# Kernel tuning notes

Measured on AMD Instinct MI355X. Metric: run time of the kernel, lower is better.

## Reference

```python
import jax, jax.numpy as jnp
import numpy as np

N = 100_000   # nodes
E = 1_600_000 # edges
IN = 128
OUT = 64
L = 3         # n_layers


def setup_inputs() -> dict:
    key = jax.random.key(0)
    ks = jax.random.split(key, 4)
    x = jax.random.normal(ks[0], (N, IN), dtype=jnp.float32)
    edge_index = jax.random.randint(ks[1], (2, E), 0, N, dtype=jnp.int64)
    # Glorot-ish init like torch Linear default
    s0 = 1.0 / np.sqrt(IN)
    W0 = jax.random.uniform(ks[2], (IN, OUT), jnp.float32, -s0, s0)
    b0 = jnp.zeros((OUT,), jnp.float32)
    so = 1.0 / np.sqrt(OUT)
    Ws = jax.random.uniform(ks[3], (L - 1, OUT, OUT), jnp.float32, -so, so)
    bs = jnp.zeros((L - 1, OUT), jnp.float32)
    return {"x": x, "edge_index": edge_index, "W0": W0, "b0": b0, "Ws": Ws, "bs": bs}


def _gcn_conv(x, src, dst, norm, W, b):
    # dense transform then degree-normalized scatter-add over edges (incl. self-loops)
    h = x @ W                                  # [N, out]
    msg = h[src] * norm[:, None]               # [E+N, out]
    out = jax.ops.segment_sum(msg, dst, num_segments=N)
    return out + b


def reference(x, edge_index, W0, b0, Ws, bs):
    loops = jnp.arange(N, dtype=edge_index.dtype)
    src = jnp.concatenate([edge_index[0], loops])  # source nodes (x_j)
    dst = jnp.concatenate([edge_index[1], loops])  # aggregation targets
    # symmetric GCN normalization: deg over A+I, norm = d^-1/2[src]*d^-1/2[dst]
    deg = jax.ops.segment_sum(jnp.ones(src.shape, x.dtype), dst, num_segments=N)
    dinv = jnp.where(deg > 0, jax.lax.rsqrt(deg), jnp.zeros((), x.dtype))
    norm = dinv[src] * dinv[dst]

    x_temp = _gcn_conv(x, src, dst, norm, W0, b0)
    h = x_temp
    for i in range(L - 1):  # fixed small layer loop
        h = jax.nn.relu(_gcn_conv(h, src, dst, norm, Ws[i], bs[i]))
    return h + x_temp  # sum_res residual
```

## Files before the change

kernel.cpp:

```cpp
#include <hip/hip_runtime.h>


#define LB 8
#define BKN 256
#define CHUNK 4096
#define EPT 16
#define CAP 8192
#define PADS 3
#define CAPCOL (CAP + BKN * PADS)

typedef unsigned short ushort_t;
typedef __attribute__((ext_vector_type(8))) short bf16x8;
typedef __attribute__((ext_vector_type(4))) float f32x4;

__device__ __forceinline__ unsigned f2bf(float f) {
    unsigned u = __builtin_bit_cast(unsigned, f);
    return (u + 0x7FFFu + ((u >> 16) & 1u)) >> 16;
}
__device__ __forceinline__ float bf2f(ushort_t h) {
    unsigned u = ((unsigned)h) << 16;
    return __builtin_bit_cast(float, u);
}
__device__ __forceinline__ float bflo(unsigned u) {
    return __builtin_bit_cast(float, u << 16);
}
__device__ __forceinline__ float bfhi(unsigned u) {
    return __builtin_bit_cast(float, u & 0xFFFF0000u);
}

__device__ int detect_f64(const int* ei, int E, int* sflag) {
    if (threadIdx.x == 0) *sflag = 0;
    __syncthreads();
    const unsigned* raw = (const unsigned*)ei;
    int dwords = min(2 * E, 512);
    int any = 0;
    for (int i = threadIdx.x; i < dwords; i += blockDim.x)
        if ((i & 1) && raw[i]) any = 1;
    if (any) atomicOr(sflag, 1);
    __syncthreads();
    return !*sflag;
}

__global__ __launch_bounds__(256) void k_scatter(
        const int* __restrict__ ei, int E,
        int* __restrict__ bucketCursor, unsigned int* __restrict__ packed) {
    __shared__ int hist[512];
    __shared__ int base[512];
    __shared__ int sflag;
    int f64 = detect_f64(ei, E, &sflag);
    int b0 = blockIdx.x * CHUNK;
    int n = min(CHUNK, E - b0);
    int tid = threadIdx.x;
    for (int i = tid; i < 512; i += 256) hist[i] = 0;
    __syncthreads();
    int dreg[EPT], sreg[EPT];
#pragma unroll
    for (int i = 0; i < EPT; i++) {
        int idx = tid + i * 256;
        if (idx < n) {
            int e = b0 + idx;
            dreg[i] = f64 ? ei[2 * (E + e)] : ei[E + e];
            sreg[i] = f64 ? ei[2 * e] : ei[e];
            atomicAdd(&hist[dreg[i] >> LB], 1);
        }
    }
    __syncthreads();
    for (int i = tid; i < 512; i += 256) {
        int c = hist[i];
        base[i] = c ? atomicAdd(&bucketCursor[i], c) : 0;
        hist[i] = 0;
    }
    __syncthreads();
#pragma unroll
    for (int i = 0; i < EPT; i++) {
        int idx = tid + i * 256;
        if (idx < n) {
            int bk = dreg[i] >> LB;
            int pos = bk * CAP + base[bk] + atomicAdd(&hist[bk], 1);
            packed[pos] = ((unsigned)sreg[i] << LB) | (unsigned)(dreg[i] & (BKN - 1));
        }
    }
}

__global__ __launch_bounds__(256) void k_sort(
        const unsigned int* __restrict__ packed, const int* __restrict__ bucketCursor,
        int* __restrict__ col, int2* __restrict__ rp2, float* __restrict__ dinv,
        ushort_t* __restrict__ hs, int N) {
    __shared__ int hist[BKN];
    __shared__ int s[BKN];
    __shared__ int cur[BKN];
    int tid = threadIdx.x;
    int b = blockIdx.x;
    int start = b * CAP;
    int end = start + bucketCursor[b];
    hist[tid] = 0;
    __syncthreads();
    for (int e = start + tid; e < end; e += 256)
        atomicAdd(&hist[packed[e] & (BKN - 1)], 1);
    __syncthreads();
    int v = hist[tid];
    int pv = (v + PADS) & ~PADS;
    s[tid] = pv;
    __syncthreads();
    for (int off = 1; off < 256; off <<= 1) {
        int x = (tid >= off) ? s[tid - off] : 0;
        __syncthreads();
        if (tid >= off) s[tid] += x;
        __syncthreads();
    }
    int excl = s[tid] - pv;
    int st = b * CAPCOL + excl;
    cur[tid] = st;
    int node = (b << LB) + tid;
    if (node < N) {
        rp2[node] = make_int2(st, st + pv);
        dinv[node] = rsqrtf((float)(v + 1));
        for (int i = v; i < pv; i++) col[st + i] = N;
    }
    if (b == 0 && tid < 64) hs[(size_t)N * 64 + tid] = 0;
    __syncthreads();
    for (int e = start + tid; e < end; e += 256) {
        unsigned pvk = packed[e];
        int pos = atomicAdd(&cur[pvk & (BKN - 1)], 1);
        col[pos] = (int)(pvk >> LB);
    }
}

__global__ __launch_bounds__(256) void k_gemm1(
        const float* __restrict__ A, const float* __restrict__ W,
        const float* __restrict__ dinv, ushort_t* __restrict__ out, int nrows) {
    const int K = 128;
    __shared__ ushort_t sWT[64 * (K + 8)];
    int tid = threadIdx.x;
    for (int i = tid; i < K * 64; i += 256) {
        int n = i & 63, k = i >> 6;
        sWT[n * (K + 8) + k] = (ushort_t)f2bf(W[i]);
    }
    __syncthreads();
    int wave = tid >> 6, lane = tid & 63;
    int quad = lane >> 4, l16 = lane & 15;
    int rowBase = blockIdx.x * 128 + wave * 32;
    f32x4 acc[2][4];
#pragma unroll
    for (int r = 0; r < 2; r++)
#pragma unroll
        for (int c = 0; c < 4; c++) acc[r][c] = (f32x4){0.f, 0.f, 0.f, 0.f};
#pragma unroll
    for (int chunk = 0; chunk < K / 32; chunk++) {
        bf16x8 afr[2];
#pragma unroll
        for (int r = 0; r < 2; r++) {
            int row = rowBase + r * 16 + l16;
            if (row >= nrows) row = nrows - 1;
            const float* ap = A + (size_t)row * K + chunk * 32 + quad * 8;
            float4 v0 = *(const float4*)ap;
            float4 v1 = *(const float4*)(ap + 4);
            bf16x8 a;
            a[0] = (short)f2bf(v0.x); a[1] = (short)f2bf(v0.y);
            a[2] = (short)f2bf(v0.z); a[3] = (short)f2bf(v0.w);
            a[4] = (short)f2bf(v1.x); a[5] = (short)f2bf(v1.y);
            a[6] = (short)f2bf(v1.z); a[7] = (short)f2bf(v1.w);
            afr[r] = a;
        }
#pragma unroll
        for (int c = 0; c < 4; c++) {
            bf16x8 bfr = __builtin_bit_cast(
                bf16x8,
                *(const uint4*)&sWT[(c * 16 + l16) * (K + 8) + chunk * 32 + quad * 8]);
#pragma unroll
            for (int r = 0; r < 2; r++)
                acc[r][c] = __builtin_amdgcn_mfma_f32_16x16x32_bf16(
                    afr[r], bfr, acc[r][c], 0, 0, 0);
        }
    }
#pragma unroll
    for (int r = 0; r < 2; r++)
#pragma unroll
        for (int i = 0; i < 4; i++) {
            int row = rowBase + r * 16 + quad * 4 + i;
            if (row < nrows) {
                float sc = dinv[row];
#pragma unroll
                for (int c = 0; c < 4; c++)
                    out[(size_t)row * 64 + c * 16 + l16] =
                        (ushort_t)f2bf(acc[r][c][i] * sc);
            }
        }
}

__global__ __launch_bounds__(256) void k_gemm64(
        const ushort_t* __restrict__ A, const float* __restrict__ W,
        const float* __restrict__ dinv, ushort_t* __restrict__ out, int nrows) {
    const int K = 64;
    __shared__ ushort_t sWT[64 * (K + 8)];
    int tid = threadIdx.x;
    for (int i = tid; i < K * 64; i += 256) {
        int n = i & 63, k = i >> 6;
        sWT[n * (K + 8) + k] = (ushort_t)f2bf(W[i]);
    }
    __syncthreads();
    int wave = tid >> 6, lane = tid & 63;
    int quad = lane >> 4, l16 = lane & 15;
    int rowBase = blockIdx.x * 128 + wave * 32;
    f32x4 acc[2][4];
#pragma unroll
    for (int r = 0; r < 2; r++)
#pragma unroll
        for (int c = 0; c < 4; c++) acc[r][c] = (f32x4){0.f, 0.f, 0.f, 0.f};
#pragma unroll
    for (int chunk = 0; chunk < K / 32; chunk++) {
        bf16x8 afr[2];
#pragma unroll
        for (int r = 0; r < 2; r++) {
            int row = rowBase + r * 16 + l16;
            if (row >= nrows) row = nrows - 1;
            const ushort_t* ap = A + (size_t)row * K + chunk * 32 + quad * 8;
            afr[r] = __builtin_bit_cast(bf16x8, *(const uint4*)ap);
        }
#pragma unroll
        for (int c = 0; c < 4; c++) {
            bf16x8 bfr = __builtin_bit_cast(
                bf16x8,
                *(const uint4*)&sWT[(c * 16 + l16) * (K + 8) + chunk * 32 + quad * 8]);
#pragma unroll
            for (int r = 0; r < 2; r++)
                acc[r][c] = __builtin_amdgcn_mfma_f32_16x16x32_bf16(
                    afr[r], bfr, acc[r][c], 0, 0, 0);
        }
    }
#pragma unroll
    for (int r = 0; r < 2; r++)
#pragma unroll
        for (int i = 0; i < 4; i++) {
            int row = rowBase + r * 16 + quad * 4 + i;
            if (row < nrows) {
                float sc = dinv[row];
#pragma unroll
                for (int c = 0; c < 4; c++)
                    out[(size_t)row * 64 + c * 16 + l16] =
                        (ushort_t)f2bf(acc[r][c][i] * sc);
            }
        }
}

template <int RELU, int F32OUT>
__global__ __launch_bounds__(256) void k_agg4e(
        const ushort_t* __restrict__ hs, const float* __restrict__ dinv,
        const float* __restrict__ bias, const int* __restrict__ col,
        const int2* __restrict__ rp2, const ushort_t* __restrict__ residb,
        float* __restrict__ outf, ushort_t* __restrict__ outb, int n) {
    int node = (int)((blockIdx.x * blockDim.x + threadIdx.x) >> 6);
    if (node >= n) return;
    int lane = threadIdx.x & 63;
    int g = lane >> 4;
    int c4 = lane & 15;
    const ushort_t* hrow = hs + (size_t)c4 * 4;
    int2 r = rp2[node];
    int e = r.x, p = r.y;
    uint2 us = *(const uint2*)(hs + (size_t)node * 64 + c4 * 4);
    float a0 = 0.f, a1 = 0.f, a2 = 0.f, a3 = 0.f;

#define GR(m) (*(const uint2*)(hrow + (size_t)(m) * 64))
#define GACC(u)                                                             \
    a0 += bflo(u.x); a1 += bfhi(u.x);                                       \
    a2 += bflo(u.y); a3 += bfhi(u.y);

    int m0, m1, m2, m3;
    bool run = (e + 16 <= p);
    if (run) {
        m0 = col[e + g];      m1 = col[e + 4 + g];
        m2 = col[e + 8 + g];  m3 = col[e + 12 + g];
    }
    while (run) {
        uint2 u0 = GR(m0);
        uint2 u1 = GR(m1);
        uint2 u2 = GR(m2);
        uint2 u3 = GR(m3);
        e += 16;
        run = (e + 16 <= p);
        if (run) {
            m0 = col[e + g];      m1 = col[e + 4 + g];
            m2 = col[e + 8 + g];  m3 = col[e + 12 + g];
        }
        GACC(u0) GACC(u1) GACC(u2) GACC(u3)
    }
    if (p - e >= 8) {
        int t0 = col[e + g];
        int t1 = col[e + 4 + g];
        uint2 u0 = GR(t0);
        uint2 u1 = GR(t1);
        GACC(u0) GACC(u1)
        e += 8;
    }
    if (e < p) {
        int t0 = col[e + g];
        uint2 u0 = GR(t0);
        GACC(u0)
    }
#undef GR
#undef GACC

    a0 += __shfl_xor(a0, 16); a0 += __shfl_xor(a0, 32);
    a1 += __shfl_xor(a1, 16); a1 += __shfl_xor(a1, 32);
    a2 += __shfl_xor(a2, 16); a2 += __shfl_xor(a2, 32);
    a3 += __shfl_xor(a3, 16); a3 += __shfl_xor(a3, 32);

    if (lane < 16) {
        a0 += bflo(us.x); a1 += bfhi(us.x);
        a2 += bflo(us.y); a3 += bfhi(us.y);
        float sc = dinv[node];
        float4 bv = *(const float4*)(bias + c4 * 4);
        float o0 = sc * a0 + bv.x, o1 = sc * a1 + bv.y;
        float o2 = sc * a2 + bv.z, o3 = sc * a3 + bv.w;
        if (RELU) {
            o0 = fmaxf(o0, 0.f); o1 = fmaxf(o1, 0.f);
            o2 = fmaxf(o2, 0.f); o3 = fmaxf(o3, 0.f);
        }
        if (F32OUT) {
            uint2 rb = *(const uint2*)(residb + (size_t)node * 64 + c4 * 4);
            o0 += bflo(rb.x); o1 += bfhi(rb.x);
            o2 += bflo(rb.y); o3 += bfhi(rb.y);
            *(float4*)(outf + (size_t)node * 64 + c4 * 4) =
                make_float4(o0, o1, o2, o3);
        } else {
            unsigned w0 = f2bf(o0) | (f2bf(o1) << 16);
            unsigned w1 = f2bf(o2) | (f2bf(o3) << 16);
            *(uint2*)(outb + (size_t)node * 64 + c4 * 4) = make_uint2(w0, w1);
        }
    }
}

extern "C" void kernel_launch(void* const* d_in, const int* in_sizes, int n_in,
                              void* d_out, int out_size, void* d_ws, size_t ws_size,
                              hipStream_t stream) {
    const float* x  = (const float*)d_in[0];
    const int*   ei = (const int*)d_in[1];
    const float* W0 = (const float*)d_in[2];
    const float* b0 = (const float*)d_in[3];
    const float* Ws = (const float*)d_in[4];
    const float* bs = (const float*)d_in[5];
    float* out = (float*)d_out;

    const int N = in_sizes[0] / 128;
    const int E = in_sizes[1] / 2;
    const int B = (N + BKN - 1) >> LB;

    char* p = (char*)d_ws;
    auto carve = [&](size_t bytes) {
        char* r = p;
        p += (bytes + 255) & ~(size_t)255;
        return r;
    };
    int*      bucketCursor = (int*)carve(512 * 4);
    unsigned* packed       = (unsigned*)carve((size_t)B * CAP * 4);
    int*      col          = (int*)carve(((size_t)B * CAPCOL + 64) * 4);
    int2*     rp2          = (int2*)carve((size_t)N * 8);
    float*    dinv         = (float*)carve((size_t)N * 4);
    ushort_t* hs           = (ushort_t*)carve((size_t)(N + 1) * 64 * 2);
    ushort_t* xtb          = (ushort_t*)carve((size_t)N * 64 * 2);
    ushort_t* hb           = (ushort_t*)carve((size_t)N * 64 * 2);

    hipMemsetAsync(bucketCursor, 0, 512 * 4, stream);

    k_scatter<<<(E + CHUNK - 1) / CHUNK, 256, 0, stream>>>(ei, E, bucketCursor, packed);
    k_sort<<<B, 256, 0, stream>>>(packed, bucketCursor, col, rp2, dinv, hs, N);

    int gb = (N + 127) / 128;
    int ablocks = (N + 3) / 4;

    k_gemm1<<<gb, 256, 0, stream>>>(x, W0, dinv, hs, N);
    k_agg4e<0, 0><<<ablocks, 256, 0, stream>>>(hs, dinv, b0, col, rp2,
                                               nullptr, nullptr, xtb, N);
    k_gemm64<<<gb, 256, 0, stream>>>(xtb, Ws, dinv, hs, N);
    k_agg4e<1, 0><<<ablocks, 256, 0, stream>>>(hs, dinv, bs, col, rp2,
                                               nullptr, nullptr, hb, N);
    k_gemm64<<<gb, 256, 0, stream>>>(hb, Ws + 64 * 64, dinv, hs, N);
    k_agg4e<1, 1><<<ablocks, 256, 0, stream>>>(hs, dinv, bs + 64, col, rp2,
                                               xtb, out, nullptr, N);
}
```

Before: 294.2 us.

## Split node features into four 16-column planes and aggregate per plane

```diff
diff --git a/kernel.cpp b/kernel.cpp
--- a/kernel.cpp
+++ b/kernel.cpp
@@ -6,8 +6,6 @@
 #define CHUNK 4096
 #define EPT 16
 #define CAP 8192
-#define PADS 3
-#define CAPCOL (CAP + BKN * PADS)
 
 typedef unsigned short ushort_t;
 typedef __attribute__((ext_vector_type(8))) short bf16x8;
@@ -99,8 +97,7 @@
         atomicAdd(&hist[packed[e] & (BKN - 1)], 1);
     __syncthreads();
     int v = hist[tid];
-    int pv = (v + PADS) & ~PADS;
-    s[tid] = pv;
+    s[tid] = v;
     __syncthreads();
     for (int off = 1; off < 256; off <<= 1) {
         int x = (tid >= off) ? s[tid - off] : 0;
@@ -108,16 +105,17 @@
         if (tid >= off) s[tid] += x;
         __syncthreads();
     }
-    int excl = s[tid] - pv;
-    int st = b * CAPCOL + excl;
+    int st = b * CAP + s[tid] - v;
     cur[tid] = st;
     int node = (b << LB) + tid;
     if (node < N) {
-        rp2[node] = make_int2(st, st + pv);
+        rp2[node] = make_int2(st, st + v);
         dinv[node] = rsqrtf((float)(v + 1));
-        for (int i = v; i < pv; i++) col[st + i] = N;
-    }
-    if (b == 0 && tid < 64) hs[(size_t)N * 64 + tid] = 0;
+    }
+    if (b == 0 && tid < 64) {
+        size_t ns = (size_t)N + 1;
+        hs[((size_t)(tid >> 4) * ns + N) * 16 + (tid & 15)] = 0;
+    }
     __syncthreads();
     for (int e = start + tid; e < end; e += 256) {
         unsigned pvk = packed[e];
@@ -130,6 +128,7 @@
         const float* __restrict__ A, const float* __restrict__ W,
         const float* __restrict__ dinv, ushort_t* __restrict__ out, int nrows) {
     const int K = 128;
+    size_t ns = (size_t)nrows + 1;
     __shared__ ushort_t sWT[64 * (K + 8)];
     int tid = threadIdx.x;
     for (int i = tid; i < K * 64; i += 256) {
@@ -182,7 +181,7 @@
                 float sc = dinv[row];
 #pragma unroll
                 for (int c = 0; c < 4; c++)
-                    out[(size_t)row * 64 + c * 16 + l16] =
+                    out[((size_t)c * ns + row) * 16 + l16] =
                         (ushort_t)f2bf(acc[r][c][i] * sc);
             }
         }
@@ -192,6 +191,7 @@
         const ushort_t* __restrict__ A, const float* __restrict__ W,
         const float* __restrict__ dinv, ushort_t* __restrict__ out, int nrows) {
     const int K = 64;
+    size_t ns = (size_t)nrows + 1;
     __shared__ ushort_t sWT[64 * (K + 8)];
     int tid = threadIdx.x;
     for (int i = tid; i < K * 64; i += 256) {
@@ -210,11 +210,13 @@
 #pragma unroll
     for (int chunk = 0; chunk < K / 32; chunk++) {
         bf16x8 afr[2];
+        int sub = chunk * 2 + (quad >> 1);
+        int off = (quad & 1) * 8;
 #pragma unroll
         for (int r = 0; r < 2; r++) {
             int row = rowBase + r * 16 + l16;
             if (row >= nrows) row = nrows - 1;
-            const ushort_t* ap = A + (size_t)row * K + chunk * 32 + quad * 8;
+            const ushort_t* ap = A + ((size_t)sub * ns + row) * 16 + off;
             afr[r] = __builtin_bit_cast(bf16x8, *(const uint4*)ap);
         }
 #pragma unroll
@@ -237,79 +239,66 @@
                 float sc = dinv[row];
 #pragma unroll
                 for (int c = 0; c < 4; c++)
-                    out[(size_t)row * 64 + c * 16 + l16] =
+                    out[((size_t)c * ns + row) * 16 + l16] =
                         (ushort_t)f2bf(acc[r][c][i] * sc);
             }
         }
 }
 
 template <int RELU, int F32OUT>
-__global__ __launch_bounds__(256) void k_agg4e(
+__global__ __launch_bounds__(256) void k_agg16(
         const ushort_t* __restrict__ hs, const float* __restrict__ dinv,
         const float* __restrict__ bias, const int* __restrict__ col,
         const int2* __restrict__ rp2, const ushort_t* __restrict__ residb,
         float* __restrict__ outf, ushort_t* __restrict__ outb, int n) {
-    int node = (int)((blockIdx.x * blockDim.x + threadIdx.x) >> 6);
-    if (node >= n) return;
+    size_t ns = (size_t)n + 1;
+    int bid = blockIdx.x;
+    int f = bid & 3;
+    int wid = threadIdx.x >> 6;
     int lane = threadIdx.x & 63;
-    int g = lane >> 4;
-    int c4 = lane & 15;
-    const ushort_t* hrow = hs + (size_t)c4 * 4;
-    int2 r = rp2[node];
+    int nl = lane >> 4;
+    int g = (lane >> 2) & 3;
+    int c = lane & 3;
+    int node = (bid >> 2) * 16 + wid * 4 + nl;
+    const ushort_t* sub = hs + (size_t)f * ns * 16;
+
+    int2 r = rp2[node < n ? node : n - 1];
     int e = r.x, p = r.y;
-    uint2 us = *(const uint2*)(hs + (size_t)node * 64 + c4 * 4);
+    if (node >= n) { e = 0; p = 0; }
+    uint2 us = *(const uint2*)(sub + (size_t)(node < n ? node : 0) * 16 + c * 4);
     float a0 = 0.f, a1 = 0.f, a2 = 0.f, a3 = 0.f;
 
-#define GR(m) (*(const uint2*)(hrow + (size_t)(m) * 64))
+#define GR(m) (*(const uint2*)(sub + (size_t)(m) * 16 + c * 4))
 #define GACC(u)                                                             \
     a0 += bflo(u.x); a1 += bfhi(u.x);                                       \
     a2 += bflo(u.y); a3 += bfhi(u.y);
 
-    int m0, m1, m2, m3;
-    bool run = (e + 16 <= p);
-    if (run) {
-        m0 = col[e + g];      m1 = col[e + 4 + g];
-        m2 = col[e + 8 + g];  m3 = col[e + 12 + g];
-    }
-    while (run) {
+    bool any = __any(e < p);
+    int cv0 = 0, cv1 = 0;
+    if (any) { cv0 = col[e + g]; cv1 = col[e + 4 + g]; }
+    while (any) {
+        int m0 = (e + g < p) ? cv0 : n;
+        int m1 = (e + 4 + g < p) ? cv1 : n;
         uint2 u0 = GR(m0);
         uint2 u1 = GR(m1);
-        uint2 u2 = GR(m2);
-        uint2 u3 = GR(m3);
-        e += 16;
-        run = (e + 16 <= p);
-        if (run) {
-            m0 = col[e + g];      m1 = col[e + 4 + g];
-            m2 = col[e + 8 + g];  m3 = col[e + 12 + g];
-        }
-        GACC(u0) GACC(u1) GACC(u2) GACC(u3)
-    }
-    if (p - e >= 8) {
-        int t0 = col[e + g];
-        int t1 = col[e + 4 + g];
-        uint2 u0 = GR(t0);
-        uint2 u1 = GR(t1);
+        e += 8;
+        any = __any(e < p);
+        if (any) { cv0 = col[e + g]; cv1 = col[e + 4 + g]; }
         GACC(u0) GACC(u1)
-        e += 8;
-    }
-    if (e < p) {
-        int t0 = col[e + g];
-        uint2 u0 = GR(t0);
-        GACC(u0)
     }
 #undef GR
 #undef GACC
 
-    a0 += __shfl_xor(a0, 16); a0 += __shfl_xor(a0, 32);
-    a1 += __shfl_xor(a1, 16); a1 += __shfl_xor(a1, 32);
-    a2 += __shfl_xor(a2, 16); a2 += __shfl_xor(a2, 32);
-    a3 += __shfl_xor(a3, 16); a3 += __shfl_xor(a3, 32);
-
-    if (lane < 16) {
+    a0 += __shfl_xor(a0, 4); a0 += __shfl_xor(a0, 8);
+    a1 += __shfl_xor(a1, 4); a1 += __shfl_xor(a1, 8);
+    a2 += __shfl_xor(a2, 4); a2 += __shfl_xor(a2, 8);
+    a3 += __shfl_xor(a3, 4); a3 += __shfl_xor(a3, 8);
+
+    if (g == 0 && node < n) {
         a0 += bflo(us.x); a1 += bfhi(us.x);
         a2 += bflo(us.y); a3 += bfhi(us.y);
         float sc = dinv[node];
-        float4 bv = *(const float4*)(bias + c4 * 4);
+        float4 bv = *(const float4*)(bias + f * 16 + c * 4);
         float o0 = sc * a0 + bv.x, o1 = sc * a1 + bv.y;
         float o2 = sc * a2 + bv.z, o3 = sc * a3 + bv.w;
         if (RELU) {
@@ -317,15 +306,16 @@
             o2 = fmaxf(o2, 0.f); o3 = fmaxf(o3, 0.f);
         }
         if (F32OUT) {
-            uint2 rb = *(const uint2*)(residb + (size_t)node * 64 + c4 * 4);
+            uint2 rb = *(const uint2*)(residb + ((size_t)f * ns + node) * 16 + c * 4);
             o0 += bflo(rb.x); o1 += bfhi(rb.x);
             o2 += bflo(rb.y); o3 += bfhi(rb.y);
-            *(float4*)(outf + (size_t)node * 64 + c4 * 4) =
+            *(float4*)(outf + (size_t)node * 64 + f * 16 + c * 4) =
                 make_float4(o0, o1, o2, o3);
         } else {
             unsigned w0 = f2bf(o0) | (f2bf(o1) << 16);
             unsigned w1 = f2bf(o2) | (f2bf(o3) << 16);
-            *(uint2*)(outb + (size_t)node * 64 + c4 * 4) = make_uint2(w0, w1);
+            *(uint2*)(outb + ((size_t)f * ns + node) * 16 + c * 4) =
+                make_uint2(w0, w1);
         }
     }
 }
@@ -353,12 +343,12 @@
     };
     int*      bucketCursor = (int*)carve(512 * 4);
     unsigned* packed       = (unsigned*)carve((size_t)B * CAP * 4);
-    int*      col          = (int*)carve(((size_t)B * CAPCOL + 64) * 4);
+    int*      col          = (int*)carve(((size_t)B * CAP + 128) * 4);
     int2*     rp2          = (int2*)carve((size_t)N * 8);
     float*    dinv         = (float*)carve((size_t)N * 4);
     ushort_t* hs           = (ushort_t*)carve((size_t)(N + 1) * 64 * 2);
-    ushort_t* xtb          = (ushort_t*)carve((size_t)N * 64 * 2);
-    ushort_t* hb           = (ushort_t*)carve((size_t)N * 64 * 2);
+    ushort_t* xtb          = (ushort_t*)carve((size_t)(N + 1) * 64 * 2);
+    ushort_t* hb           = (ushort_t*)carve((size_t)(N + 1) * 64 * 2);
 
     hipMemsetAsync(bucketCursor, 0, 512 * 4, stream);
 
@@ -366,15 +356,15 @@
     k_sort<<<B, 256, 0, stream>>>(packed, bucketCursor, col, rp2, dinv, hs, N);
 
     int gb = (N + 127) / 128;
-    int ablocks = (N + 3) / 4;
+    int ablocks = ((N + 15) / 16) * 4;
 
     k_gemm1<<<gb, 256, 0, stream>>>(x, W0, dinv, hs, N);
-    k_agg4e<0, 0><<<ablocks, 256, 0, stream>>>(hs, dinv, b0, col, rp2,
+    k_agg16<0, 0><<<ablocks, 256, 0, stream>>>(hs, dinv, b0, col, rp2,
                                                nullptr, nullptr, xtb, N);
     k_gemm64<<<gb, 256, 0, stream>>>(xtb, Ws, dinv, hs, N);
-    k_agg4e<1, 0><<<ablocks, 256, 0, stream>>>(hs, dinv, bs, col, rp2,
+    k_agg16<1, 0><<<ablocks, 256, 0, stream>>>(hs, dinv, bs, col, rp2,
                                                nullptr, nullptr, hb, N);
     k_gemm64<<<gb, 256, 0, stream>>>(hb, Ws + 64 * 64, dinv, hs, N);
-    k_agg4e<1, 1><<<ablocks, 256, 0, stream>>>(hs, dinv, bs + 64, col, rp2,
+    k_agg16<1, 1><<<ablocks, 256, 0, stream>>>(hs, dinv, bs + 64, col, rp2,
                                                xtb, out, nullptr, N);
 }
```

Result: slower. 314.3 us (+6.8%).

## Process two nodes per wave in aggregation and keep sort keys in registers

Applied to the files above, without the earlier changes.

```diff
diff --git a/kernel.cpp b/kernel.cpp
--- a/kernel.cpp
+++ b/kernel.cpp
@@ -5,6 +5,7 @@
 #define BKN 256
 #define CHUNK 4096
 #define EPT 16
+#define SEPT 20
 #define CAP 8192
 #define PADS 3
 #define CAPCOL (CAP + BKN * PADS)
@@ -92,11 +93,25 @@
     int tid = threadIdx.x;
     int b = blockIdx.x;
     int start = b * CAP;
-    int end = start + bucketCursor[b];
+    int cnt = bucketCursor[b];
+    int end = start + cnt;
+    int inreg = (cnt <= 256 * SEPT);
+    unsigned preg[SEPT];
     hist[tid] = 0;
     __syncthreads();
-    for (int e = start + tid; e < end; e += 256)
-        atomicAdd(&hist[packed[e] & (BKN - 1)], 1);
+    if (inreg) {
+#pragma unroll
+        for (int i = 0; i < SEPT; i++) {
+            int e = start + tid + i * 256;
+            if (e < end) {
+                preg[i] = packed[e];
+                atomicAdd(&hist[preg[i] & (BKN - 1)], 1);
+            }
+        }
+    } else {
+        for (int e = start + tid; e < end; e += 256)
+            atomicAdd(&hist[packed[e] & (BKN - 1)], 1);
+    }
     __syncthreads();
     int v = hist[tid];
     int pv = (v + PADS) & ~PADS;
@@ -119,10 +134,22 @@
     }
     if (b == 0 && tid < 64) hs[(size_t)N * 64 + tid] = 0;
     __syncthreads();
-    for (int e = start + tid; e < end; e += 256) {
-        unsigned pvk = packed[e];
-        int pos = atomicAdd(&cur[pvk & (BKN - 1)], 1);
-        col[pos] = (int)(pvk >> LB);
+    if (inreg) {
+#pragma unroll
+        for (int i = 0; i < SEPT; i++) {
+            int e = start + tid + i * 256;
+            if (e < end) {
+                unsigned pvk = preg[i];
+                int pos = atomicAdd(&cur[pvk & (BKN - 1)], 1);
+                col[pos] = (int)(pvk >> LB);
+            }
+        }
+    } else {
+        for (int e = start + tid; e < end; e += 256) {
+            unsigned pvk = packed[e];
+            int pos = atomicAdd(&cur[pvk & (BKN - 1)], 1);
+            col[pos] = (int)(pvk >> LB);
+        }
     }
 }
 
@@ -244,88 +271,157 @@
 }
 
 template <int RELU, int F32OUT>
-__global__ __launch_bounds__(256) void k_agg4e(
+__global__ __launch_bounds__(256) void k_agg2n(
         const ushort_t* __restrict__ hs, const float* __restrict__ dinv,
         const float* __restrict__ bias, const int* __restrict__ col,
         const int2* __restrict__ rp2, const ushort_t* __restrict__ residb,
         float* __restrict__ outf, ushort_t* __restrict__ outb, int n) {
-    int node = (int)((blockIdx.x * blockDim.x + threadIdx.x) >> 6);
-    if (node >= n) return;
+    int gw = (int)((blockIdx.x * blockDim.x + threadIdx.x) >> 6);
+    int node0 = gw << 1, node1 = node0 | 1;
+    if (node0 >= n) return;
     int lane = threadIdx.x & 63;
     int g = lane >> 4;
     int c4 = lane & 15;
+    bool has1 = node1 < n;
     const ushort_t* hrow = hs + (size_t)c4 * 4;
-    int2 r = rp2[node];
-    int e = r.x, p = r.y;
-    uint2 us = *(const uint2*)(hs + (size_t)node * 64 + c4 * 4);
-    float a0 = 0.f, a1 = 0.f, a2 = 0.f, a3 = 0.f;
+    uint2 us0 = *(const uint2*)(hs + (size_t)node0 * 64 + c4 * 4);
+    uint2 us1 = has1 ? *(const uint2*)(hs + (size_t)node1 * 64 + c4 * 4)
+                     : make_uint2(0u, 0u);
+    float sc0 = dinv[node0];
+    float sc1 = has1 ? dinv[node1] : 0.f;
+    int2 r0 = rp2[node0];
+    int2 r1 = has1 ? rp2[node1] : make_int2(0, 0);
+    int e0 = r0.x, p0 = r0.y;
+    int e1 = r1.x, p1 = r1.y;
+    float A0 = 0.f, A1 = 0.f, A2 = 0.f, A3 = 0.f;
+    float B0 = 0.f, B1 = 0.f, B2 = 0.f, B3 = 0.f;
 
 #define GR(m) (*(const uint2*)(hrow + (size_t)(m) * 64))
-#define GACC(u)                                                             \
-    a0 += bflo(u.x); a1 += bfhi(u.x);                                       \
-    a2 += bflo(u.y); a3 += bfhi(u.y);
-
-    int m0, m1, m2, m3;
-    bool run = (e + 16 <= p);
-    if (run) {
-        m0 = col[e + g];      m1 = col[e + 4 + g];
-        m2 = col[e + 8 + g];  m3 = col[e + 12 + g];
-    }
-    while (run) {
-        uint2 u0 = GR(m0);
-        uint2 u1 = GR(m1);
-        uint2 u2 = GR(m2);
-        uint2 u3 = GR(m3);
-        e += 16;
-        run = (e + 16 <= p);
-        if (run) {
-            m0 = col[e + g];      m1 = col[e + 4 + g];
-            m2 = col[e + 8 + g];  m3 = col[e + 12 + g];
-        }
-        GACC(u0) GACC(u1) GACC(u2) GACC(u3)
-    }
-    if (p - e >= 8) {
-        int t0 = col[e + g];
-        int t1 = col[e + 4 + g];
-        uint2 u0 = GR(t0);
-        uint2 u1 = GR(t1);
-        GACC(u0) GACC(u1)
-        e += 8;
-    }
-    if (e < p) {
-        int t0 = col[e + g];
-        uint2 u0 = GR(t0);
-        GACC(u0)
-    }
+#define GACCA(u)                                                            \
+    A0 += bflo(u.x); A1 += bfhi(u.x); A2 += bflo(u.y); A3 += bfhi(u.y);
+#define GACCB(u)                                                            \
+    B0 += bflo(u.x); B1 += bfhi(u.x); B2 += bflo(u.y); B3 += bfhi(u.y);
+
+    while (p0 - e0 > 32) {
+        int d0 = col[e0 + g],      d1 = col[e0 + 4 + g];
+        int d2 = col[e0 + 8 + g],  d3 = col[e0 + 12 + g];
+        int d4 = col[e0 + 16 + g], d5 = col[e0 + 20 + g];
+        int d6 = col[e0 + 24 + g], d7 = col[e0 + 28 + g];
+        uint2 v0 = GR(d0), v1 = GR(d1), v2 = GR(d2), v3 = GR(d3);
+        uint2 v4 = GR(d4), v5 = GR(d5), v6 = GR(d6), v7 = GR(d7);
+        GACCA(v0) GACCA(v1) GACCA(v2) GACCA(v3)
+        GACCA(v4) GACCA(v5) GACCA(v6) GACCA(v7)
+        e0 += 32;
+    }
+    while (p1 - e1 > 32) {
+        int d0 = col[e1 + g],      d1 = col[e1 + 4 + g];
+        int d2 = col[e1 + 8 + g],  d3 = col[e1 + 12 + g];
+        int d4 = col[e1 + 16 + g], d5 = col[e1 + 20 + g];
+        int d6 = col[e1 + 24 + g], d7 = col[e1 + 28 + g];
+        uint2 v0 = GR(d0), v1 = GR(d1), v2 = GR(d2), v3 = GR(d3);
+        uint2 v4 = GR(d4), v5 = GR(d5), v6 = GR(d6), v7 = GR(d7);
+        GACCB(v0) GACCB(v1) GACCB(v2) GACCB(v3)
+        GACCB(v4) GACCB(v5) GACCB(v6) GACCB(v7)
+        e1 += 32;
+    }
+    int rem0 = p0 - e0, rem1 = p1 - e1;
+    bool t0 = rem0 > 16, t1 = rem1 > 16;
+    int c00 = col[e0 + g],     c01 = col[e0 + 4 + g];
+    int c02 = col[e0 + 8 + g], c03 = col[e0 + 12 + g];
+    int c10 = col[e1 + g],     c11 = col[e1 + 4 + g];
+    int c12 = col[e1 + 8 + g], c13 = col[e1 + 12 + g];
+    int c04 = 0, c05 = 0, c06 = 0, c07 = 0;
+    int c14 = 0, c15 = 0, c16 = 0, c17 = 0;
+    if (t0) {
+        c04 = col[e0 + 16 + g]; c05 = col[e0 + 20 + g];
+        c06 = col[e0 + 24 + g]; c07 = col[e0 + 28 + g];
+    }
+    if (t1) {
+        c14 = col[e1 + 16 + g]; c15 = col[e1 + 20 + g];
+        c16 = col[e1 + 24 + g]; c17 = col[e1 + 28 + g];
+    }
+    int m00 = (g < rem0)      ? c00 : n;
+    int m01 = (4 + g < rem0)  ? c01 : n;
+    int m02 = (8 + g < rem0)  ? c02 : n;
+    int m03 = (12 + g < rem0) ? c03 : n;
+    int m10 = (g < rem1)      ? c10 : n;
+    int m11 = (4 + g < rem1)  ? c11 : n;
+    int m12 = (8 + g < rem1)  ? c12 : n;
+    int m13 = (12 + g < rem1) ? c13 : n;
+    uint2 u00 = GR(m00), u01 = GR(m01), u02 = GR(m02), u03 = GR(m03);
+    uint2 u10 = GR(m10), u11 = GR(m11), u12 = GR(m12), u13 = GR(m13);
+    if (t0) {
+        int m04 = (16 + g < rem0) ? c04 : n;
+        int m05 = (20 + g < rem0) ? c05 : n;
+        int m06 = (24 + g < rem0) ? c06 : n;
+        int m07 = (28 + g < rem0) ? c07 : n;
+        uint2 u04 = GR(m04), u05 = GR(m05), u06 = GR(m06), u07 = GR(m07);
+        GACCA(u04) GACCA(u05) GACCA(u06) GACCA(u07)
+    }
+    if (t1) {
+        int m14 = (16 + g < rem1) ? c14 : n;
+        int m15 = (20 + g < rem1) ? c15 : n;
+        int m16 = (24 + g < rem1) ? c16 : n;
+        int m17 = (28 + g < rem1) ? c17 : n;
+        uint2 u14 = GR(m14), u15 = GR(m15), u16 = GR(m16), u17 = GR(m17);
+        GACCB(u14) GACCB(u15) GACCB(u16) GACCB(u17)
+    }
+    GACCA(u00) GACCA(u01) GACCA(u02) GACCA(u03)
+    GACCB(u10) GACCB(u11) GACCB(u12) GACCB(u13)
 #undef GR
-#undef GACC
-
-    a0 += __shfl_xor(a0, 16); a0 += __shfl_xor(a0, 32);
-    a1 += __shfl_xor(a1, 16); a1 += __shfl_xor(a1, 32);
-    a2 += __shfl_xor(a2, 16); a2 += __shfl_xor(a2, 32);
-    a3 += __shfl_xor(a3, 16); a3 += __shfl_xor(a3, 32);
+#undef GACCA
+#undef GACCB
+
+    A0 += __shfl_xor(A0, 16); A0 += __shfl_xor(A0, 32);
+    A1 += __shfl_xor(A1, 16); A1 += __shfl_xor(A1, 32);
+    A2 += __shfl_xor(A2, 16); A2 += __shfl_xor(A2, 32);
+    A3 += __shfl_xor(A3, 16); A3 += __shfl_xor(A3, 32);
+    B0 += __shfl_xor(B0, 16); B0 += __shfl_xor(B0, 32);
+    B1 += __shfl_xor(B1, 16); B1 += __shfl_xor(B1, 32);
+    B2 += __shfl_xor(B2, 16); B2 += __shfl_xor(B2, 32);
+    B3 += __shfl_xor(B3, 16); B3 += __shfl_xor(B3, 32);
 
     if (lane < 16) {
-        a0 += bflo(us.x); a1 += bfhi(us.x);
-        a2 += bflo(us.y); a3 += bfhi(us.y);
-        float sc = dinv[node];
+        float o0 = A0 + bflo(us0.x), o1 = A1 + bfhi(us0.x);
+        float o2 = A2 + bflo(us0.y), o3 = A3 + bfhi(us0.y);
         float4 bv = *(const float4*)(bias + c4 * 4);
-        float o0 = sc * a0 + bv.x, o1 = sc * a1 + bv.y;
-        float o2 = sc * a2 + bv.z, o3 = sc * a3 + bv.w;
+        o0 = sc0 * o0 + bv.x; o1 = sc0 * o1 + bv.y;
+        o2 = sc0 * o2 + bv.z; o3 = sc0 * o3 + bv.w;
         if (RELU) {
             o0 = fmaxf(o0, 0.f); o1 = fmaxf(o1, 0.f);
             o2 = fmaxf(o2, 0.f); o3 = fmaxf(o3, 0.f);
         }
         if (F32OUT) {
-            uint2 rb = *(const uint2*)(residb + (size_t)node * 64 + c4 * 4);
+            uint2 rb = *(const uint2*)(residb + (size_t)node0 * 64 + c4 * 4);
             o0 += bflo(rb.x); o1 += bfhi(rb.x);
             o2 += bflo(rb.y); o3 += bfhi(rb.y);
-            *(float4*)(outf + (size_t)node * 64 + c4 * 4) =
+            *(float4*)(outf + (size_t)node0 * 64 + c4 * 4) =
                 make_float4(o0, o1, o2, o3);
         } else {
             unsigned w0 = f2bf(o0) | (f2bf(o1) << 16);
             unsigned w1 = f2bf(o2) | (f2bf(o3) << 16);
-            *(uint2*)(outb + (size_t)node * 64 + c4 * 4) = make_uint2(w0, w1);
+            *(uint2*)(outb + (size_t)node0 * 64 + c4 * 4) = make_uint2(w0, w1);
+        }
+    } else if (lane < 32 && has1) {
+        float o0 = B0 + bflo(us1.x), o1 = B1 + bfhi(us1.x);
+        float o2 = B2 + bflo(us1.y), o3 = B3 + bfhi(us1.y);
+        float4 bv = *(const float4*)(bias + c4 * 4);
+        o0 = sc1 * o0 + bv.x; o1 = sc1 * o1 + bv.y;
+        o2 = sc1 * o2 + bv.z; o3 = sc1 * o3 + bv.w;
+        if (RELU) {
+            o0 = fmaxf(o0, 0.f); o1 = fmaxf(o1, 0.f);
+            o2 = fmaxf(o2, 0.f); o3 = fmaxf(o3, 0.f);
+        }
+        if (F32OUT) {
+            uint2 rb = *(const uint2*)(residb + (size_t)node1 * 64 + c4 * 4);
+            o0 += bflo(rb.x); o1 += bfhi(rb.x);
+            o2 += bflo(rb.y); o3 += bfhi(rb.y);
+            *(float4*)(outf + (size_t)node1 * 64 + c4 * 4) =
+                make_float4(o0, o1, o2, o3);
+        } else {
+            unsigned w0 = f2bf(o0) | (f2bf(o1) << 16);
+            unsigned w1 = f2bf(o2) | (f2bf(o3) << 16);
+            *(uint2*)(outb + (size_t)node1 * 64 + c4 * 4) = make_uint2(w0, w1);
         }
     }
 }
@@ -366,15 +462,15 @@
     k_sort<<<B, 256, 0, stream>>>(packed, bucketCursor, col, rp2, dinv, hs, N);
 
     int gb = (N + 127) / 128;
-    int ablocks = (N + 3) / 4;
+    int ablocks = (N + 7) / 8;
 
     k_gemm1<<<gb, 256, 0, stream>>>(x, W0, dinv, hs, N);
-    k_agg4e<0, 0><<<ablocks, 256, 0, stream>>>(hs, dinv, b0, col, rp2,
+    k_agg2n<0, 0><<<ablocks, 256, 0, stream>>>(hs, dinv, b0, col, rp2,
                                                nullptr, nullptr, xtb, N);
     k_gemm64<<<gb, 256, 0, stream>>>(xtb, Ws, dinv, hs, N);
-    k_agg4e<1, 0><<<ablocks, 256, 0, stream>>>(hs, dinv, bs, col, rp2,
+    k_agg2n<1, 0><<<ablocks, 256, 0, stream>>>(hs, dinv, bs, col, rp2,
                                                nullptr, nullptr, hb, N);
     k_gemm64<<<gb, 256, 0, stream>>>(hb, Ws + 64 * 64, dinv, hs, N);
-    k_agg4e<1, 1><<<ablocks, 256, 0, stream>>>(hs, dinv, bs + 64, col, rp2,
+    k_agg2n<1, 1><<<ablocks, 256, 0, stream>>>(hs, dinv, bs + 64, col, rp2,
                                                xtb, out, nullptr, N);
 }
```

After: 290.5 us. Within noise of the previous version (-1.3%).
